# Optimization experiments

Measured on AMD Instinct MI355X. Metric: run time of the kernel, lower is better.

Reference implementation:

```python
import jax, jax.numpy as jnp
import numpy as np

D_MODEL, D_STATE, D_CONV, EXPAND, DT_RANK = 1024, 16, 4, 2, 32
D_INNER = D_MODEL * EXPAND


def setup_inputs() -> dict:
    key = jax.random.key(0)
    ks = jax.random.split(key, 12)
    B, T = 4, 2048
    s_in = 1.0 / np.sqrt(D_MODEL)
    s_dt = 1.0 / np.sqrt(DT_RANK)
    s_out = 1.0 / np.sqrt(D_INNER)
    return {
        "x": jax.random.normal(ks[0], (B, T, D_MODEL), jnp.float32),
        "Wi": jax.random.uniform(ks[1], (2 * D_INNER, D_MODEL), jnp.float32, -s_in, s_in),
        "bi": jax.random.uniform(ks[2], (2 * D_INNER,), jnp.float32, -s_in, s_in),
        "conv_w": jax.random.uniform(ks[3], (D_INNER, 1, D_CONV), jnp.float32, -0.5, 0.5),
        "conv_b": jax.random.uniform(ks[4], (D_INNER,), jnp.float32, -0.5, 0.5),
        "Wdt": jax.random.uniform(ks[5], (D_INNER, DT_RANK), jnp.float32, -s_dt, s_dt),
        "bdt": jax.random.uniform(ks[6], (D_INNER,), jnp.float32, -s_dt, s_dt),
        "A_log": jnp.log(0.99 - jax.random.uniform(ks[7], (D_INNER, D_STATE), jnp.float32) * 0.01),
        "Bm": jax.random.normal(ks[8], (D_INNER, D_STATE), jnp.float32) * 0.01,
        "Cm": jax.random.normal(ks[9], (D_INNER, D_STATE), jnp.float32) * 0.01,
        "Dv": jnp.ones((D_INNER,), jnp.float32) * 0.1,
        "Wo": jax.random.uniform(ks[10], (D_MODEL, D_INNER), jnp.float32, -s_out, s_out),
        "bo": jax.random.uniform(ks[11], (D_MODEL,), jnp.float32, -s_out, s_out),
    }


def _ssm_forward(x, Wi, bi, conv_w, conv_b, Wdt, bdt, A_log, Bm, Cm, Dv, Wo, bo):
    Bb, T, _ = x.shape
    xz = x @ Wi.T + bi                      # [B,T,2*d_inner]
    x_in, z = xz[..., :D_INNER], xz[..., D_INNER:]
    # depthwise causal conv (torch pads both sides by d_conv-1 then slices [:T] == left-pad only)
    xc = jnp.transpose(x_in, (0, 2, 1))     # [B,d_inner,T]
    xc = jax.lax.conv_general_dilated(
        xc, conv_w, (1,), [(D_CONV - 1, 0)],
        dimension_numbers=("NCH", "OIH", "NCH"), feature_group_count=D_INNER)
    xc = xc + conv_b[None, :, None]
    u = jax.nn.silu(jnp.transpose(xc, (0, 2, 1)))  # [B,T,d_inner]
    dt = jax.nn.softplus(x_in[..., :DT_RANK] @ Wdt.T + bdt)  # [B,T,d_inner]
    A = -jnp.exp(A_log)                     # [d_inner,d_state]

    def step(h, inp):
        dt_t, u_t = inp                     # each [B,d_inner]
        h = h * jnp.exp(dt_t[:, :, None] * A[None]) + dt_t[:, :, None] * Bm[None] * u_t[:, :, None]
        y = jnp.einsum("bdn,dn->bd", h, Cm)
        return h, y

    h0 = jnp.zeros((Bb, D_INNER, D_STATE), x.dtype)
    _, ys = jax.lax.scan(step, h0, (jnp.swapaxes(dt, 0, 1), jnp.swapaxes(u, 0, 1)))
    out = jnp.swapaxes(ys, 0, 1) * jax.nn.silu(z)
    return out @ Wo.T + bo + x * Dv.mean()


def reference(x, Wi, bi, conv_w, conv_b, Wdt, bdt, A_log, Bm, Cm, Dv, Wo, bo):
    return _ssm_forward(x, Wi, bi, conv_w, conv_b, Wdt, bdt, A_log, Bm, Cm, Dv, Wo, bo)
```

## Files before the change

kernel.cpp:

```cpp
#include <hip/hip_runtime.h>
#include <hip/hip_bf16.h>
#include <math.h>
#include <stdint.h>


using bf16 = __hip_bfloat16;
typedef __attribute__((ext_vector_type(8))) __bf16 bf16x8;
typedef __attribute__((ext_vector_type(4))) float f32x4;

static constexpr int Bdim = 4;
static constexpr int Tdim = 2048;
static constexpr int DM   = 1024;
static constexpr int DI   = 2048;
static constexpr int DS   = 16;
static constexpr int DC   = 4;
static constexpr int DTR  = 32;
static constexpr int Mrows = Bdim * Tdim;
static constexpr int P    = 32;
static constexpr int TC2  = Tdim / P;
static constexpr float LOG2E = 1.44269504f;

__device__ __forceinline__ float b2f(bf16 v) { return __bfloat162float(v); }
__device__ __forceinline__ bf16  f2b(float v) { return __float2bfloat16(v); }
__device__ __forceinline__ float silu_f(float v) { return v / (1.0f + __expf(-v)); }
__device__ __forceinline__ float softplus_f(float v) {
  return (v > 15.0f) ? v : __logf(1.0f + __expf(v));
}
__device__ __forceinline__ float bfbits2f(unsigned short u) {
  return __uint_as_float((unsigned)u << 16);
}
__device__ __forceinline__ float exp2_f(float v) {
  return __builtin_amdgcn_exp2f(v);
}

#define GLOAD_LDS16(gp, lp)                                                  \
  __builtin_amdgcn_global_load_lds(                                          \
      (const __attribute__((address_space(1))) uint32_t*)(gp),               \
      (__attribute__((address_space(3))) uint32_t*)(lp), 16, 0, 0)

__global__ __launch_bounds__(256)
void kmean(const float* __restrict__ Dv, float* __restrict__ meanp) {
  __shared__ float red[256];
  float s = 0.0f;
  for (int i = threadIdx.x; i < DI; i += 256) s += Dv[i];
  red[threadIdx.x] = s;
  __syncthreads();
  for (int o = 128; o > 0; o >>= 1) {
    if (threadIdx.x < o) red[threadIdx.x] += red[threadIdx.x + o];
    __syncthreads();
  }
  if (threadIdx.x == 0) *meanp = red[0] / (float)DI;
}

__device__ __forceinline__ unsigned pack2(float x, float y) {
  return (unsigned)__builtin_bit_cast(unsigned short, f2b(x)) |
         ((unsigned)__builtin_bit_cast(unsigned short, f2b(y)) << 16);
}
__global__ __launch_bounds__(256)
void kcvt(const float* __restrict__ src, bf16* __restrict__ dst, int n8) {
  const int i = blockIdx.x * 256 + threadIdx.x;
  if (i >= n8) return;
  const float4 a = reinterpret_cast<const float4*>(src)[2 * i];
  const float4 b = reinterpret_cast<const float4*>(src)[2 * i + 1];
  uint4 v;
  v.x = pack2(a.x, a.y); v.y = pack2(a.z, a.w);
  v.z = pack2(b.x, b.y); v.w = pack2(b.z, b.w);
  reinterpret_cast<uint4*>(dst)[i] = v;
}

__global__ __launch_bounds__(256)
void k1(const bf16* __restrict__ A, const bf16* __restrict__ W,
        const float* __restrict__ bi,
        bf16* __restrict__ XIN, bf16* __restrict__ ZG)
{
  __shared__ bf16 Al[128 * 32];
  __shared__ bf16 Bl[128 * 32];
  const int tid  = threadIdx.x;
  const int bm   = blockIdx.y * 128;
  const int bn   = blockIdx.x * 128;
  const int lane = tid & 63, wid = tid >> 6;
  const int wr = wid >> 1, wc = wid & 1;
  const int fr = lane & 15;
  const int kg = (lane >> 4) * 8;
  const int ldr = tid >> 2, ldc = (tid & 3) * 8;
  constexpr int K = DM;

  const bf16* ga = A + (size_t)(bm + ldr) * K + ldc;
  const bf16* gb = W + (size_t)(bn + ldr) * K + ldc;

  f32x4 acc[4][4];
#pragma unroll
  for (int i = 0; i < 4; ++i)
#pragma unroll
    for (int j = 0; j < 4; ++j) acc[i][j] = (f32x4){0.f, 0.f, 0.f, 0.f};

  for (int k0 = 0; k0 < K; k0 += 32) {
    GLOAD_LDS16(ga + k0,          &Al[tid * 8]);
    GLOAD_LDS16(ga + k0 + 64 * K, &Al[2048 + tid * 8]);
    GLOAD_LDS16(gb + k0,          &Bl[tid * 8]);
    GLOAD_LDS16(gb + k0 + 64 * K, &Bl[2048 + tid * 8]);
    asm volatile("s_waitcnt vmcnt(0)" ::: "memory");
    __syncthreads();
    bf16x8 af[4], bfr[4];
#pragma unroll
    for (int i = 0; i < 4; ++i)
      af[i]  = *(const bf16x8*)&Al[(wr * 64 + i * 16 + fr) * 32 + kg];
#pragma unroll
    for (int j = 0; j < 4; ++j)
      bfr[j] = *(const bf16x8*)&Bl[(wc * 64 + j * 16 + fr) * 32 + kg];
#pragma unroll
    for (int i = 0; i < 4; ++i)
#pragma unroll
      for (int j = 0; j < 4; ++j)
        acc[i][j] = __builtin_amdgcn_mfma_f32_16x16x32_bf16(
            af[i], bfr[j], acc[i][j], 0, 0, 0);
    __syncthreads();
  }

  const int r0 = (lane >> 4) * 4;
#pragma unroll
  for (int j = 0; j < 4; ++j) {
    const int col = bn + wc * 64 + j * 16 + fr;
    const float bv = bi[col];
    const bool isx = (col < DI);
#pragma unroll
    for (int i = 0; i < 4; ++i) {
      const int rowb = bm + wr * 64 + i * 16 + r0;
#pragma unroll
      for (int r = 0; r < 4; ++r) {
        const float v = acc[i][j][r] + bv;
        if (isx) XIN[(size_t)(rowb + r) * DI + col]        = f2b(v);
        else     ZG [(size_t)(rowb + r) * DI + (col - DI)] = f2b(silu_f(v));
      }
    }
  }
}

__global__ __launch_bounds__(256)
void kscanA(const bf16* __restrict__ XIN, const bf16* __restrict__ WDTB,
            const float* __restrict__ cw, const float* __restrict__ cb,
            const float* __restrict__ bdt,
            const float* __restrict__ A_log, const float* __restrict__ Bm,
            float* __restrict__ APROD, float* __restrict__ HEND,
            float2* __restrict__ DFg)
{
  __shared__ float xc[67][20];
  __shared__ float dts[16][68];
  __shared__ float fs [16][68];

  const int tid  = threadIdx.x;
  const int lane = tid & 63;
  const int wid  = tid >> 6;
  const int n  = tid & 15;
  const int dl = tid >> 4;
  const int d0 = blockIdx.x * 16;
  const int d  = d0 + dl;
  const int row0 = blockIdx.y * 64;
  const int b  = row0 >> 11;
  const size_t rbase = (size_t)b * Tdim;
  const int t0 = row0 - (int)rbase;

  const int fr = lane & 15;
  const int kg = (lane >> 4) * 8;
  const float bdtf = bdt[d0 + fr];
  const bf16x8 wfrag = *(const bf16x8*)&WDTB[(size_t)(d0 + fr) * DTR + kg];

  const float Af2 = -__expf(A_log[(size_t)d * DS + n]) * LOG2E;
  const float Bf  = Bm[(size_t)d * DS + n];
  const float w0 = cw[d * DC + 0], w1 = cw[d * DC + 1];
  const float w2 = cw[d * DC + 2], w3 = cw[d * DC + 3];
  const float c0 = cb[d];

  for (int e = tid; e < 67 * 4; e += 256) {
    const int i = e >> 2, p4 = (e & 3) * 4;
    const int rr = t0 + i - 3;
    float4 v;
    if (rr < 0) {
      v = make_float4(0.f, 0.f, 0.f, 0.f);
    } else {
      const ushort4 u =
          *(const ushort4*)&XIN[(rbase + rr) * DI + d0 + p4];
      v = make_float4(bfbits2f(u.x), bfbits2f(u.y), bfbits2f(u.z), bfbits2f(u.w));
    }
    *(float4*)&xc[i][p4] = v;
  }
  {
    const bf16x8 xfrag =
        *(const bf16x8*)&XIN[(rbase + t0 + wid * 16 + fr) * DI + kg];
    f32x4 a = (f32x4){0.f, 0.f, 0.f, 0.f};
    a = __builtin_amdgcn_mfma_f32_16x16x32_bf16(xfrag, wfrag, a, 0, 0, 0);
    float4 dq;
    dq.x = softplus_f(a[0] + bdtf);
    dq.y = softplus_f(a[1] + bdtf);
    dq.z = softplus_f(a[2] + bdtf);
    dq.w = softplus_f(a[3] + bdtf);
    *(float4*)&dts[fr][wid * 16 + (lane >> 4) * 4] = dq;
  }
  __syncthreads();

#pragma unroll
  for (int q = 0; q < 4; ++q) {
    const int tl = n + 16 * q;
    const float cv = c0 + w0 * xc[tl][dl] + w1 * xc[tl + 1][dl]
                        + w2 * xc[tl + 2][dl] + w3 * xc[tl + 3][dl];
    const float uv  = silu_f(cv);
    fs[dl][tl] = dts[dl][tl] * uv;
  }
  __syncthreads();

  for (int e = tid; e < 64 * 16; e += 256) {
    const int tl = e >> 4, dd = e & 15;
    DFg[(size_t)(row0 + tl) * DI + d0 + dd] =
        make_float2(dts[dd][tl], fs[dd][tl]);
  }

  float acc = 0.0f;
  float R   = 0.0f;
#pragma unroll 4
  for (int sq = 15; sq >= 0; --sq) {
    const float4 dv = *(const float4*)&dts[dl][4 * sq];
    const float4 fv = *(const float4*)&fs [dl][4 * sq];
#define ASTEP(DT, FF)                                                         \
    {                                                                         \
      acc += exp2_f(R * Af2) * (Bf * (FF));                                   \
      R += (DT);                                                              \
    }
    ASTEP(dv.w, fv.w); ASTEP(dv.z, fv.z); ASTEP(dv.y, fv.y); ASTEP(dv.x, fv.x);
#undef ASTEP
  }

  const size_t si = (size_t)blockIdx.y * DI * DS + (size_t)d * DS + n;
  APROD[si] = exp2_f(R * Af2);
  HEND [si] = acc;
}

__global__ __launch_bounds__(256)
void kscanH(const float* __restrict__ APROD, const float* __restrict__ HEND,
            float* __restrict__ HINIT)
{
  const int idx = blockIdx.x * 256 + threadIdx.x;
  const int b  = idx / (DI * DS);
  const int dn = idx % (DI * DS);
  float H = 0.0f;
#pragma unroll
  for (int c = 0; c < P; ++c) {
    const size_t si = (size_t)(b * P + c) * DI * DS + dn;
    HINIT[si] = H;
    H = APROD[si] * H + HEND[si];
  }
}

__global__ __launch_bounds__(256, 4)
void kscanB(const float2* __restrict__ DFg, bf16* __restrict__ ZG,
            const float* __restrict__ A_log, const float* __restrict__ Bm,
            const float* __restrict__ Cm, const float* __restrict__ HINIT)
{
  const int tid  = threadIdx.x;
  const int cg   = blockIdx.x >> 3;
  const int d    = ((blockIdx.x & 7) << 8) + tid;
  const int row0 = cg * 64;

  float A2[DS], Bc[DS], Cc[DS], h[DS];
#pragma unroll
  for (int nn = 0; nn < DS; ++nn) {
    A2[nn] = -__expf(A_log[(size_t)d * DS + nn]) * LOG2E;
    Bc[nn] = Bm[(size_t)d * DS + nn];
    Cc[nn] = Cm[(size_t)d * DS + nn];
    h [nn] = HINIT[(size_t)cg * DI * DS + (size_t)d * DS + nn];
  }

  const float2* dfp = DFg + (size_t)row0 * DI + d;
  bf16* zp = ZG + (size_t)row0 * DI + d;

#pragma unroll 4
  for (int t = 0; t < TC2; ++t) {
    const float2 df = dfp[(size_t)t * DI];
    float y = 0.0f;
#pragma unroll
    for (int nn = 0; nn < DS; ++nn) {
      const float e = exp2_f(df.x * A2[nn]);
      h[nn] = h[nn] * e + Bc[nn] * df.y;
      y += h[nn] * Cc[nn];
    }
    bf16* zt = zp + (size_t)t * DI;
    *zt = f2b(y * b2f(*zt));
  }
}

__global__ __launch_bounds__(256)
void k2(const bf16* __restrict__ G, const bf16* __restrict__ W,
        const float* __restrict__ x, const float* __restrict__ bo,
        const float* __restrict__ meanp, float* __restrict__ out)
{
  __shared__ bf16 Al[128 * 32];
  __shared__ bf16 Bl[128 * 32];
  const int tid  = threadIdx.x;
  const int bm   = blockIdx.y * 128;
  const int bn   = blockIdx.x * 128;
  const int lane = tid & 63, wid = tid >> 6;
  const int wr = wid >> 1, wc = wid & 1;
  const int fr = lane & 15;
  const int kg = (lane >> 4) * 8;
  const int ldr = tid >> 2, ldc = (tid & 3) * 8;
  constexpr int K = DI;

  const bf16* ga = G + (size_t)(bm + ldr) * K + ldc;
  const bf16* gb = W + (size_t)(bn + ldr) * K + ldc;
  const float mv = *meanp;

  f32x4 acc[4][4];
#pragma unroll
  for (int i = 0; i < 4; ++i)
#pragma unroll
    for (int j = 0; j < 4; ++j) acc[i][j] = (f32x4){0.f, 0.f, 0.f, 0.f};

  for (int k0 = 0; k0 < K; k0 += 32) {
    GLOAD_LDS16(ga + k0,          &Al[tid * 8]);
    GLOAD_LDS16(ga + k0 + 64 * K, &Al[2048 + tid * 8]);
    GLOAD_LDS16(gb + k0,          &Bl[tid * 8]);
    GLOAD_LDS16(gb + k0 + 64 * K, &Bl[2048 + tid * 8]);
    asm volatile("s_waitcnt vmcnt(0)" ::: "memory");
    __syncthreads();
    bf16x8 af[4], bfr[4];
#pragma unroll
    for (int i = 0; i < 4; ++i)
      af[i]  = *(const bf16x8*)&Al[(wr * 64 + i * 16 + fr) * 32 + kg];
#pragma unroll
    for (int j = 0; j < 4; ++j)
      bfr[j] = *(const bf16x8*)&Bl[(wc * 64 + j * 16 + fr) * 32 + kg];
#pragma unroll
    for (int i = 0; i < 4; ++i)
#pragma unroll
      for (int j = 0; j < 4; ++j)
        acc[i][j] = __builtin_amdgcn_mfma_f32_16x16x32_bf16(
            af[i], bfr[j], acc[i][j], 0, 0, 0);
    __syncthreads();
  }

  const int r0 = (lane >> 4) * 4;
#pragma unroll
  for (int j = 0; j < 4; ++j) {
    const int col = bn + wc * 64 + j * 16 + fr;
    const float bv = bo[col];
#pragma unroll
    for (int i = 0; i < 4; ++i) {
      const int rowb = bm + wr * 64 + i * 16 + r0;
#pragma unroll
      for (int r = 0; r < 4; ++r) {
        const size_t oi = (size_t)(rowb + r) * DM + col;
        out[oi] = acc[i][j][r] + bv + mv * x[oi];
      }
    }
  }
}

extern "C" void kernel_launch(void* const* d_in, const int* in_sizes, int n_in,
                              void* d_out, int out_size, void* d_ws, size_t ws_size,
                              hipStream_t stream)
{
  const float* x    = (const float*)d_in[0];
  const float* Wi   = (const float*)d_in[1];
  const float* bi   = (const float*)d_in[2];
  const float* cw   = (const float*)d_in[3];
  const float* cb   = (const float*)d_in[4];
  const float* Wdt  = (const float*)d_in[5];
  const float* bdt  = (const float*)d_in[6];
  const float* Alog = (const float*)d_in[7];
  const float* Bm   = (const float*)d_in[8];
  const float* Cm   = (const float*)d_in[9];
  const float* Dv   = (const float*)d_in[10];
  const float* Wo   = (const float*)d_in[11];
  const float* bo   = (const float*)d_in[12];
  float* out = (float*)d_out;

  char* ws = (char*)d_ws;
  float*  MEANP = (float*)(ws);
  bf16*   WOB   = (bf16*)(ws + 256);
  bf16*   XIN   = (bf16*)(ws + 4194560);
  bf16*   ZG    = (bf16*)(ws + 37748992);
  float*  APROD = (float*)(ws + 71303424);
  float*  HEND  = (float*)(ws + 88080640);
  float*  HINIT = (float*)(ws + 104857856);
  bf16*   WDTB  = (bf16*)(ws + 121635072);
  float2* DFg   = (float2*)(ws + 121766144);
  bf16*   XB    = (bf16*)(ws + 121766144);
  bf16*   WIB   = (bf16*)(ws + 138543360);

  kmean<<<1, 256, 0, stream>>>(Dv, MEANP);
  kcvt<<<Mrows * DM / 8 / 256, 256, 0, stream>>>(x,  XB,  Mrows * DM / 8);
  kcvt<<<2 * DI * DM / 8 / 256, 256, 0, stream>>>(Wi, WIB, 2 * DI * DM / 8);
  kcvt<<<DM * DI / 8 / 256, 256, 0, stream>>>(Wo, WOB, DM * DI / 8);
  kcvt<<<DI * DTR / 8 / 256, 256, 0, stream>>>(Wdt, WDTB, DI * DTR / 8);

  k1<<<dim3(2 * DI / 128, Mrows / 128), 256, 0, stream>>>(XB, WIB, bi, XIN, ZG);

  kscanA<<<dim3(DI / 16, Mrows / 64), 256, 0, stream>>>(
      XIN, WDTB, cw, cb, bdt, Alog, Bm, APROD, HEND, DFg);
  kscanH<<<dim3(Bdim * DI * DS / 256), 256, 0, stream>>>(APROD, HEND, HINIT);
  kscanB<<<dim3(Mrows / 64 * 8), 256, 0, stream>>>(
      DFg, ZG, Alog, Bm, Cm, HINIT);

  k2<<<dim3(DM / 128, Mrows / 128), 256, 0, stream>>>(ZG, WOB, x, bo, MEANP, out);
}
```

Measured before the change: 427.0 us.

## Recompute dt and conv in both scan passes instead of materializing DFg

After: 451.7 us. +5.8%, slower.

```diff
diff --git a/kernel.cpp b/kernel.cpp
--- a/kernel.cpp
+++ b/kernel.cpp
@@ -136,102 +136,123 @@
   }
 }
 
-__global__ __launch_bounds__(256)
-void kscanA(const bf16* __restrict__ XIN, const bf16* __restrict__ WDTB,
-            const float* __restrict__ cw, const float* __restrict__ cb,
-            const float* __restrict__ bdt,
-            const float* __restrict__ A_log, const float* __restrict__ Bm,
-            float* __restrict__ APROD, float* __restrict__ HEND,
-            float2* __restrict__ DFg)
-{
-  __shared__ float xc[67][20];
-  __shared__ float dts[16][68];
-  __shared__ float fs [16][68];
-
-  const int tid  = threadIdx.x;
-  const int lane = tid & 63;
-  const int wid  = tid >> 6;
-  const int n  = tid & 15;
-  const int dl = tid >> 4;
-  const int d0 = blockIdx.x * 16;
-  const int d  = d0 + dl;
-  const int row0 = blockIdx.y * 64;
-  const int b  = row0 >> 11;
-  const size_t rbase = (size_t)b * Tdim;
-  const int t0 = row0 - (int)rbase;
-
-  const int fr = lane & 15;
-  const int kg = (lane >> 4) * 8;
-  const float bdtf = bdt[d0 + fr];
-  const bf16x8 wfrag = *(const bf16x8*)&WDTB[(size_t)(d0 + fr) * DTR + kg];
-
-  const float Af2 = -__expf(A_log[(size_t)d * DS + n]) * LOG2E;
-  const float Bf  = Bm[(size_t)d * DS + n];
-  const float w0 = cw[d * DC + 0], w1 = cw[d * DC + 1];
-  const float w2 = cw[d * DC + 2], w3 = cw[d * DC + 3];
-  const float c0 = cb[d];
-
-  for (int e = tid; e < 67 * 4; e += 256) {
-    const int i = e >> 2, p4 = (e & 3) * 4;
-    const int rr = t0 + i - 3;
-    float4 v;
-    if (rr < 0) {
-      v = make_float4(0.f, 0.f, 0.f, 0.f);
-    } else {
-      const ushort4 u =
-          *(const ushort4*)&XIN[(rbase + rr) * DI + d0 + p4];
-      v = make_float4(bfbits2f(u.x), bfbits2f(u.y), bfbits2f(u.z), bfbits2f(u.w));
-    }
-    *(float4*)&xc[i][p4] = v;
-  }
-  {
-    const bf16x8 xfrag =
-        *(const bf16x8*)&XIN[(rbase + t0 + wid * 16 + fr) * DI + kg];
-    f32x4 a = (f32x4){0.f, 0.f, 0.f, 0.f};
-    a = __builtin_amdgcn_mfma_f32_16x16x32_bf16(xfrag, wfrag, a, 0, 0, 0);
-    float4 dq;
-    dq.x = softplus_f(a[0] + bdtf);
-    dq.y = softplus_f(a[1] + bdtf);
-    dq.z = softplus_f(a[2] + bdtf);
-    dq.w = softplus_f(a[3] + bdtf);
-    *(float4*)&dts[fr][wid * 16 + (lane >> 4) * 4] = dq;
-  }
-  __syncthreads();
-
+#define SCAN_PROLOG(NEED_C)                                                   \
+  const int tid  = threadIdx.x;                                               \
+  const int lane = tid & 63;                                                  \
+  const int w    = tid >> 6;                                                  \
+  const int dbase = blockIdx.x * 256 + w * 64;                                \
+  const int d_own = dbase + lane;                                             \
+  const int cg   = blockIdx.y;                                                \
+  const int row0 = cg * 64;                                                   \
+  const int tloc0 = row0 & (Tdim - 1);                                        \
+  const int fr = lane & 15, kg = (lane >> 4) * 8;                             \
+  const int jown = lane >> 4;                                                 \
+                                      \
+  bf16x8 xf[4], wf[4];                                                        \
+  _Pragma("unroll")                                                           \
+  for (int i = 0; i < 4; ++i)                                                 \
+    xf[i] = *(const bf16x8*)&XIN[(size_t)(row0 + i * 16 + fr) * DI + kg];     \
+  _Pragma("unroll")                                                           \
+  for (int j = 0; j < 4; ++j)                                                 \
+    wf[j] = *(const bf16x8*)&WDTB[(size_t)(dbase + j * 16 + fr) * DTR + kg];  \
+  f32x4 dtv[4][4];                                                            \
+  _Pragma("unroll")                                                           \
+  for (int i = 0; i < 4; ++i)                                                 \
+    _Pragma("unroll")                                                         \
+    for (int j = 0; j < 4; ++j) {                                             \
+      f32x4 z = (f32x4){0.f, 0.f, 0.f, 0.f};                                  \
+      dtv[i][j] = __builtin_amdgcn_mfma_f32_16x16x32_bf16(xf[i], wf[j], z,    \
+                                                          0, 0, 0);           \
+    }                                                                         \
+  float bj[4];                                                                \
+  _Pragma("unroll")                                                           \
+  for (int j = 0; j < 4; ++j) bj[j] = bdt[dbase + j * 16 + fr];               \
+  _Pragma("unroll")                                                           \
+  for (int i = 0; i < 4; ++i)                                                 \
+    _Pragma("unroll")                                                         \
+    for (int j = 0; j < 4; ++j)                                               \
+      _Pragma("unroll")                                                       \
+      for (int r = 0; r < 4; ++r)                                             \
+        dtv[i][j][r] = softplus_f(dtv[i][j][r] + bj[j]);                      \
+                                               \
+  float A2[DS], Bc[DS];                                                       \
+  NEED_C(float Cc[DS];)                                                       \
+  _Pragma("unroll")                                                           \
+  for (int q = 0; q < 4; ++q) {                                               \
+    const float4 al = *(const float4*)&A_log[(size_t)d_own * DS + 4 * q];     \
+    const float4 bl = *(const float4*)&Bm  [(size_t)d_own * DS + 4 * q];      \
+    A2[4 * q + 0] = -__expf(al.x) * LOG2E;                                    \
+    A2[4 * q + 1] = -__expf(al.y) * LOG2E;                                    \
+    A2[4 * q + 2] = -__expf(al.z) * LOG2E;                                    \
+    A2[4 * q + 3] = -__expf(al.w) * LOG2E;                                    \
+    Bc[4 * q + 0] = bl.x; Bc[4 * q + 1] = bl.y;                               \
+    Bc[4 * q + 2] = bl.z; Bc[4 * q + 3] = bl.w;                               \
+    NEED_C(const float4 cl = *(const float4*)&Cm[(size_t)d_own * DS + 4 * q]; \
+    Cc[4 * q + 0] = cl.x; Cc[4 * q + 1] = cl.y;                               \
+    Cc[4 * q + 2] = cl.z; Cc[4 * q + 3] = cl.w;)                              \
+  }                                                                           \
+  const float4 cwv = *(const float4*)&cw[d_own * DC];                         \
+  const float w0 = cwv.x, w1 = cwv.y, w2 = cwv.z, w3 = cwv.w;                 \
+  const float c0 = cb[d_own];                                                 \
+                                                     \
+  float x3 = (tloc0 >= 3) ? b2f(XIN[(size_t)(row0 - 3) * DI + d_own]) : 0.f;  \
+  float x2 = (tloc0 >= 2) ? b2f(XIN[(size_t)(row0 - 2) * DI + d_own]) : 0.f;  \
+  float x1 = (tloc0 >= 1) ? b2f(XIN[(size_t)(row0 - 1) * DI + d_own]) : 0.f;
+
+#define YES(...) __VA_ARGS__
+#define NO(...)
+
+#define DT_FETCH(T, OUT)                                                      \
+  {                                                                           \
+    const int srcl = (((T) & 15) >> 2) * 16 + fr;                             \
+    const float q0 = __shfl(dtv[(T) >> 4][0][(T) & 3], srcl);                 \
+    const float q1 = __shfl(dtv[(T) >> 4][1][(T) & 3], srcl);                 \
+    const float q2 = __shfl(dtv[(T) >> 4][2][(T) & 3], srcl);                 \
+    const float q3 = __shfl(dtv[(T) >> 4][3][(T) & 3], srcl);                 \
+    OUT = (jown == 0) ? q0 : (jown == 1) ? q1 : (jown == 2) ? q2 : q3;        \
+  }
+
+__global__ __launch_bounds__(256, 3)
+void kscanA2(const bf16* __restrict__ XIN, const bf16* __restrict__ WDTB,
+             const float* __restrict__ cw, const float* __restrict__ cb,
+             const float* __restrict__ bdt,
+             const float* __restrict__ A_log, const float* __restrict__ Bm,
+             float* __restrict__ APROD, float* __restrict__ HEND)
+{
+  SCAN_PROLOG(NO)
+
+  float h[DS];
+#pragma unroll
+  for (int nn = 0; nn < DS; ++nn) h[nn] = 0.0f;
+  float R = 0.0f;
+
+#pragma unroll
+  for (int t = 0; t < TC2; ++t) {
+    const float x0 = b2f(XIN[(size_t)(row0 + t) * DI + d_own]);
+    const float cv = c0 + w0 * x3 + w1 * x2 + w2 * x1 + w3 * x0;
+    const float uv = silu_f(cv);
+    float dt;
+    DT_FETCH(t, dt)
+    const float f = dt * uv;
+    R += dt;
+#pragma unroll
+    for (int nn = 0; nn < DS; ++nn)
+      h[nn] = h[nn] * exp2_f(dt * A2[nn]) + Bc[nn] * f;
+    x3 = x2; x2 = x1; x1 = x0;
+  }
+
+  float* ap = APROD + (size_t)cg * DI * DS + (size_t)d_own * DS;
+  float* hp = HEND  + (size_t)cg * DI * DS + (size_t)d_own * DS;
 #pragma unroll
   for (int q = 0; q < 4; ++q) {
-    const int tl = n + 16 * q;
-    const float cv = c0 + w0 * xc[tl][dl] + w1 * xc[tl + 1][dl]
-                        + w2 * xc[tl + 2][dl] + w3 * xc[tl + 3][dl];
-    const float uv  = silu_f(cv);
-    fs[dl][tl] = dts[dl][tl] * uv;
-  }
-  __syncthreads();
-
-  for (int e = tid; e < 64 * 16; e += 256) {
-    const int tl = e >> 4, dd = e & 15;
-    DFg[(size_t)(row0 + tl) * DI + d0 + dd] =
-        make_float2(dts[dd][tl], fs[dd][tl]);
-  }
-
-  float acc = 0.0f;
-  float R   = 0.0f;
-#pragma unroll 4
-  for (int sq = 15; sq >= 0; --sq) {
-    const float4 dv = *(const float4*)&dts[dl][4 * sq];
-    const float4 fv = *(const float4*)&fs [dl][4 * sq];
-#define ASTEP(DT, FF)                                                         \
-    {                                                                         \
-      acc += exp2_f(R * Af2) * (Bf * (FF));                                   \
-      R += (DT);                                                              \
-    }
-    ASTEP(dv.w, fv.w); ASTEP(dv.z, fv.z); ASTEP(dv.y, fv.y); ASTEP(dv.x, fv.x);
-#undef ASTEP
-  }
-
-  const size_t si = (size_t)blockIdx.y * DI * DS + (size_t)d * DS + n;
-  APROD[si] = exp2_f(R * Af2);
-  HEND [si] = acc;
+    float4 av, hv;
+    av.x = exp2_f(R * A2[4 * q + 0]); av.y = exp2_f(R * A2[4 * q + 1]);
+    av.z = exp2_f(R * A2[4 * q + 2]); av.w = exp2_f(R * A2[4 * q + 3]);
+    hv.x = h[4 * q + 0]; hv.y = h[4 * q + 1];
+    hv.z = h[4 * q + 2]; hv.w = h[4 * q + 3];
+    *(float4*)&ap[4 * q] = av;
+    *(float4*)&hp[4 * q] = hv;
+  }
 }
 
 __global__ __launch_bounds__(256)
@@ -250,40 +271,44 @@
   }
 }
 
-__global__ __launch_bounds__(256, 4)
-void kscanB(const float2* __restrict__ DFg, bf16* __restrict__ ZG,
-            const float* __restrict__ A_log, const float* __restrict__ Bm,
-            const float* __restrict__ Cm, const float* __restrict__ HINIT)
-{
-  const int tid  = threadIdx.x;
-  const int cg   = blockIdx.x >> 3;
-  const int d    = ((blockIdx.x & 7) << 8) + tid;
-  const int row0 = cg * 64;
-
-  float A2[DS], Bc[DS], Cc[DS], h[DS];
-#pragma unroll
-  for (int nn = 0; nn < DS; ++nn) {
-    A2[nn] = -__expf(A_log[(size_t)d * DS + nn]) * LOG2E;
-    Bc[nn] = Bm[(size_t)d * DS + nn];
-    Cc[nn] = Cm[(size_t)d * DS + nn];
-    h [nn] = HINIT[(size_t)cg * DI * DS + (size_t)d * DS + nn];
-  }
-
-  const float2* dfp = DFg + (size_t)row0 * DI + d;
-  bf16* zp = ZG + (size_t)row0 * DI + d;
-
-#pragma unroll 4
+__global__ __launch_bounds__(256, 3)
+void kscanB2(const bf16* __restrict__ XIN, bf16* __restrict__ ZG,
+             const bf16* __restrict__ WDTB,
+             const float* __restrict__ cw, const float* __restrict__ cb,
+             const float* __restrict__ bdt,
+             const float* __restrict__ A_log, const float* __restrict__ Bm,
+             const float* __restrict__ Cm, const float* __restrict__ HINIT)
+{
+  SCAN_PROLOG(YES)
+
+  float h[DS];
+  {
+    const float* ip = HINIT + (size_t)cg * DI * DS + (size_t)d_own * DS;
+#pragma unroll
+    for (int q = 0; q < 4; ++q) {
+      const float4 iv = *(const float4*)&ip[4 * q];
+      h[4 * q + 0] = iv.x; h[4 * q + 1] = iv.y;
+      h[4 * q + 2] = iv.z; h[4 * q + 3] = iv.w;
+    }
+  }
+
+#pragma unroll
   for (int t = 0; t < TC2; ++t) {
-    const float2 df = dfp[(size_t)t * DI];
+    const float x0 = b2f(XIN[(size_t)(row0 + t) * DI + d_own]);
+    const float cv = c0 + w0 * x3 + w1 * x2 + w2 * x1 + w3 * x0;
+    const float uv = silu_f(cv);
+    float dt;
+    DT_FETCH(t, dt)
+    const float f = dt * uv;
     float y = 0.0f;
 #pragma unroll
     for (int nn = 0; nn < DS; ++nn) {
-      const float e = exp2_f(df.x * A2[nn]);
-      h[nn] = h[nn] * e + Bc[nn] * df.y;
+      h[nn] = h[nn] * exp2_f(dt * A2[nn]) + Bc[nn] * f;
       y += h[nn] * Cc[nn];
     }
-    bf16* zt = zp + (size_t)t * DI;
+    bf16* zt = ZG + (size_t)(row0 + t) * DI + d_own;
     *zt = f2b(y * b2f(*zt));
+    x3 = x2; x2 = x1; x1 = x0;
   }
 }
 
@@ -374,17 +399,16 @@
   float* out = (float*)d_out;
 
   char* ws = (char*)d_ws;
-  float*  MEANP = (float*)(ws);
-  bf16*   WOB   = (bf16*)(ws + 256);
-  bf16*   XIN   = (bf16*)(ws + 4194560);
-  bf16*   ZG    = (bf16*)(ws + 37748992);
-  float*  APROD = (float*)(ws + 71303424);
-  float*  HEND  = (float*)(ws + 88080640);
-  float*  HINIT = (float*)(ws + 104857856);
-  bf16*   WDTB  = (bf16*)(ws + 121635072);
-  float2* DFg   = (float2*)(ws + 121766144);
-  bf16*   XB    = (bf16*)(ws + 121766144);
-  bf16*   WIB   = (bf16*)(ws + 138543360);
+  float* MEANP = (float*)(ws);
+  bf16*  WOB   = (bf16*)(ws + 256);
+  bf16*  XIN   = (bf16*)(ws + 4194560);
+  bf16*  ZG    = (bf16*)(ws + 37748992);
+  float* APROD = (float*)(ws + 71303424);
+  float* HEND  = (float*)(ws + 88080640);
+  float* HINIT = (float*)(ws + 104857856);
+  bf16*  WDTB  = (bf16*)(ws + 121635072);
+  bf16*  XB    = (bf16*)(ws + 121766144);
+  bf16*  WIB   = (bf16*)(ws + 138543360);
 
   kmean<<<1, 256, 0, stream>>>(Dv, MEANP);
   kcvt<<<Mrows * DM / 8 / 256, 256, 0, stream>>>(x,  XB,  Mrows * DM / 8);
@@ -394,11 +418,11 @@
 
   k1<<<dim3(2 * DI / 128, Mrows / 128), 256, 0, stream>>>(XB, WIB, bi, XIN, ZG);
 
-  kscanA<<<dim3(DI / 16, Mrows / 64), 256, 0, stream>>>(
-      XIN, WDTB, cw, cb, bdt, Alog, Bm, APROD, HEND, DFg);
+  kscanA2<<<dim3(DI / 256, Mrows / 64), 256, 0, stream>>>(
+      XIN, WDTB, cw, cb, bdt, Alog, Bm, APROD, HEND);
   kscanH<<<dim3(Bdim * DI * DS / 256), 256, 0, stream>>>(APROD, HEND, HINIT);
-  kscanB<<<dim3(Mrows / 64 * 8), 256, 0, stream>>>(
-      DFg, ZG, Alog, Bm, Cm, HINIT);
+  kscanB2<<<dim3(DI / 256, Mrows / 64), 256, 0, stream>>>(
+      XIN, ZG, WDTB, cw, cb, bdt, Alog, Bm, Cm, HINIT);
 
   k2<<<dim3(DM / 128, Mrows / 128), 256, 0, stream>>>(ZG, WOB, x, bo, MEANP, out);
 }
```
